# Performance work log

Hardware: AMD Instinct MI355X
Metric: run time of the kernel (lower is better)

## Reference

```python
import jax, jax.numpy as jnp
import numpy as np

EMBED_DIM = 768
NUM_HEADS = 12
HEAD_DIM = EMBED_DIM // NUM_HEADS
SCALE = HEAD_DIM ** -0.5


def setup_inputs() -> dict:
    key = jax.random.key(0)
    k_x, k_qkv, k_pw, k_pb = jax.random.split(key, 4)
    B, N = 2, 4096
    x = jax.random.normal(k_x, (B, N, EMBED_DIM), dtype=jnp.float32)
    # nn.Linear weights stored as [out, in]; we keep [in, out] for x @ W
    w_qkv = jax.random.normal(k_qkv, (EMBED_DIM, 3 * EMBED_DIM), dtype=jnp.float32) * (EMBED_DIM ** -0.5)
    w_proj = jax.random.normal(k_pw, (EMBED_DIM, EMBED_DIM), dtype=jnp.float32) * (EMBED_DIM ** -0.5)
    b_proj = jax.random.normal(k_pb, (EMBED_DIM,), dtype=jnp.float32) * 0.02
    return {"x": x, "w_qkv": w_qkv, "w_proj": w_proj, "b_proj": b_proj}


def reference(x, w_qkv, w_proj, b_proj):
    B, N, D = x.shape
    H, hd = NUM_HEADS, HEAD_DIM
    qkv = x @ w_qkv                                   # [B, N, 3*D]
    qkv = qkv.reshape(B, N, 3, H, hd)                 # matches '(qkv h d)' split order
    q, k, v = (qkv[:, :, i].transpose(0, 2, 1, 3) for i in range(3))  # each [B, H, N, hd]
    attn = jnp.einsum('bhid,bhjd->bhij', q, k) * SCALE  # [B, H, N, N] fully materialized
    attn = jax.nn.softmax(attn, axis=-1)
    out = jnp.einsum('bhij,bhjd->bhid', attn, v)        # [B, H, N, hd]
    out = out.transpose(0, 2, 1, 3).reshape(B, N, D)    # 'b h n d -> b n (h d)'
    return out @ w_proj + b_proj
```

## Files before the change

### kernel.cpp

```cpp
#include <hip/hip_runtime.h>
#include <hip/hip_bf16.h>

typedef __attribute__((ext_vector_type(4))) float f32x4;
typedef __attribute__((ext_vector_type(4))) int i32x4;
typedef __attribute__((ext_vector_type(8))) short s16x8;

static constexpr int NB = 2, NH = 12, SEQ = 4096, DM = 768, HD = 64;
static constexpr int ROWS = NB * SEQ;
static constexpr float QSC = 0.125f * 1.44269504f;

#define MFMA(a, b, c) __builtin_amdgcn_mfma_f32_16x16x32_bf16((a), (b), (c), 0, 0, 0)

typedef const void __attribute__((address_space(1)))* gas_t;
typedef void __attribute__((address_space(3)))* las_t;

__device__ __forceinline__ short f2bf(float f) {
  union { float f; unsigned u; } v; v.f = f;
  unsigned r = v.u + 0x7fffu + ((v.u >> 16) & 1u);
  return (short)(r >> 16);
}

__device__ __forceinline__ float exp2v(float x) {
  float r; asm("v_exp_f32 %0, %1" : "=v"(r) : "v"(x)); return r;
}

__global__ __launch_bounds__(256) void k_cast4(const float* __restrict__ in,
                                               short* __restrict__ out, int n4) {
  int i = blockIdx.x * 256 + threadIdx.x;
  if (i < n4) {
    float4 v = reinterpret_cast<const float4*>(in)[i];
    short4 o = { f2bf(v.x), f2bf(v.y), f2bf(v.z), f2bf(v.w) };
    reinterpret_cast<short4*>(out)[i] = o;
  }
}

__global__ __launch_bounds__(256) void k_tcast2(const float* __restrict__ in,
                                                short* __restrict__ out, int r, int c) {
  __shared__ short tile[32][33];
  int tpc = c >> 5;
  int by = blockIdx.x / tpc, bx = blockIdx.x % tpc;
  int tx = threadIdx.x & 31, ty = threadIdx.x >> 5;
#pragma unroll
  for (int i = 0; i < 4; ++i)
    tile[ty + i * 8][tx] = f2bf(in[(size_t)(by * 32 + ty + i * 8) * c + bx * 32 + tx]);
  __syncthreads();
#pragma unroll
  for (int i = 0; i < 4; ++i)
    out[(size_t)(bx * 32 + ty + i * 8) * r + by * 32 + tx] = tile[tx][ty + i * 8];
}

__device__ __forceinline__ void gemm128(const short* __restrict__ A,
                                        const short* __restrict__ Bt,
                                        int K, int row0, int col0,
                                        short As[2][4096], short Bs[2][4096],
                                        f32x4 acc[4][4]) {
  int w = threadIdx.x >> 6, l = threadIdx.x & 63;
  int q = l & 15, g = l >> 4;
  int wr = w >> 1, wc = w & 1;
  int sr = w * 16 + (l >> 2);
  int sc = (l & 3) * 8;

#define STG(buf, k0)                                                           \
  {                                                                            \
    _Pragma("unroll")                                                          \
    for (int i = 0; i < 2; ++i) {                                              \
      __builtin_amdgcn_global_load_lds(                                        \
          (gas_t)(A + (size_t)(row0 + i * 64 + sr) * K + (k0) + sc),           \
          (las_t)&As[buf][i * 2048 + w * 512], 16, 0, 0);                      \
      __builtin_amdgcn_global_load_lds(                                        \
          (gas_t)(Bt + (size_t)(col0 + i * 64 + sr) * K + (k0) + sc),          \
          (las_t)&Bs[buf][i * 2048 + w * 512], 16, 0, 0);                      \
    }                                                                          \
  }

  STG(0, 0);
  __syncthreads();
  int cur = 0;
  for (int k0 = 0; k0 < K; k0 += 32) {
    if (k0 + 32 < K) STG(cur ^ 1, k0 + 32);
    s16x8 af[4], bf[4];
#pragma unroll
    for (int m = 0; m < 4; ++m)
      af[m] = *reinterpret_cast<const s16x8*>(&As[cur][(wr * 64 + m * 16 + q) * 32 + g * 8]);
#pragma unroll
    for (int n = 0; n < 4; ++n)
      bf[n] = *reinterpret_cast<const s16x8*>(&Bs[cur][(wc * 64 + n * 16 + q) * 32 + g * 8]);
#pragma unroll
    for (int m = 0; m < 4; ++m)
#pragma unroll
      for (int n = 0; n < 4; ++n)
        acc[m][n] = MFMA(af[m], bf[n], acc[m][n]);
    __syncthreads();
    cur ^= 1;
  }
#undef STG
}

__global__ __launch_bounds__(256) void k_gemm_qkv2(const short* __restrict__ xb,
                                                   const short* __restrict__ wt,
                                                   short* __restrict__ qw,
                                                   short* __restrict__ kw,
                                                   short* __restrict__ vtw) {
  __shared__ __align__(16) short As[2][4096], Bs[2][4096];
  int bid = blockIdx.x;
  int swz = (bid & 7) * 144 + (bid >> 3);
  int brow = swz / 18, bcol = swz % 18;
  int row0 = brow * 128, col0 = bcol * 128;
  f32x4 acc[4][4] = {};
  gemm128(xb, wt, DM, row0, col0, As, Bs, acc);

  int w = threadIdx.x >> 6, l = threadIdx.x & 63;
  int q = l & 15, g = l >> 4;
  int wr = w >> 1, wc = w & 1;
  int cb = col0 + wc * 64;
  int which = cb / DM, h = (cb % DM) >> 6;
  int rowb = row0 + wr * 64;
  int b = rowb >> 12;
  int bh = b * NH + h;
#pragma unroll
  for (int m = 0; m < 4; ++m) {
#pragma unroll
    for (int n = 0; n < 4; ++n) {
      int d = n * 16 + q;
      if (which == 2) {
        int nseq = (rowb & 4095) + m * 16 + g * 4;
        short4 ov = { f2bf(acc[m][n][0]), f2bf(acc[m][n][1]),
                      f2bf(acc[m][n][2]), f2bf(acc[m][n][3]) };
        *reinterpret_cast<short4*>(&vtw[((size_t)bh * HD + d) * SEQ + nseq]) = ov;
      } else {
        short* dst = (which == 0) ? qw : kw;
        float sc = (which == 0) ? QSC : 1.f;
#pragma unroll
        for (int r = 0; r < 4; ++r) {
          int nseq = (rowb & 4095) + m * 16 + g * 4 + r;
          dst[((size_t)bh * SEQ + nseq) * HD + d] = f2bf(acc[m][n][r] * sc);
        }
      }
    }
  }
}

__global__ __launch_bounds__(256) void k_gemm_proj2(const short* __restrict__ aob,
                                                    const short* __restrict__ wt,
                                                    const float* __restrict__ bias,
                                                    float* __restrict__ out) {
  __shared__ __align__(16) short As[2][4096], Bs[2][4096];
  int bid = blockIdx.x;
  int swz = (bid & 7) * 48 + (bid >> 3);
  int brow = swz / 6, bcol = swz % 6;
  int row0 = brow * 128, col0 = bcol * 128;
  f32x4 acc[4][4] = {};
  gemm128(aob, wt, DM, row0, col0, As, Bs, acc);

  int w = threadIdx.x >> 6, l = threadIdx.x & 63;
  int q = l & 15, g = l >> 4;
  int wr = w >> 1, wc = w & 1;
#pragma unroll
  for (int m = 0; m < 4; ++m)
#pragma unroll
    for (int n = 0; n < 4; ++n) {
      int col = col0 + wc * 64 + n * 16 + q;
      float bv = bias[col];
#pragma unroll
      for (int r = 0; r < 4; ++r) {
        int row = row0 + wr * 64 + m * 16 + g * 4 + r;
        out[(size_t)row * DM + col] = acc[m][n][r] + bv;
      }
    }
}

__global__ __launch_bounds__(256, 4) void k_attn7(const short* __restrict__ qw,
                                                  const short* __restrict__ kw,
                                                  const short* __restrict__ vtw,
                                                  short* __restrict__ ao) {
  __shared__ __align__(16) short lds[2][2][4096];

  int bid = blockIdx.x;
  int swz = (bid & 7) * 96 + (bid >> 3);
  int bh = swz >> 5;
  int qchunk = swz & 31;

  int w = threadIdx.x >> 6, l = threadIdx.x & 63;
  int q = l & 15, g = l >> 4;

  const short* Kg = kw + (size_t)bh * SEQ * HD;
  const short* Vg = vtw + (size_t)bh * HD * SEQ;

  int ss = (l & 7) ^ (l >> 3) ^ ((w & 1) << 2);
  int rst = w * 8 + (l >> 3);

  int qbase = qchunk * 128 + w * 32;
  s16x8 qf[2][2];
#pragma unroll
  for (int qt2 = 0; qt2 < 2; ++qt2)
#pragma unroll
    for (int kh = 0; kh < 2; ++kh)
      qf[qt2][kh] = *reinterpret_cast<const s16x8*>(
          qw + ((size_t)bh * SEQ + qbase + qt2 * 16 + q) * HD + kh * 32 + g * 8);

  s16x8 ones;
  {
    short o1 = (q == 0) ? (short)0x3F80 : (short)0;
#pragma unroll
    for (int i = 0; i < 8; ++i) ones[i] = o1;
  }

  f32x4 o[2][4] = {};
  f32x4 lsa[2] = {};

#define STAGE(buf, t)                                                              \
  {                                                                                \
    int key0 = (t) * 64;                                                           \
    _Pragma("unroll")                                                              \
    for (int i = 0; i < 2; ++i) {                                                  \
      const short* gk = Kg + (size_t)(key0 + i * 32 + rst) * HD + ss * 8;          \
      __builtin_amdgcn_global_load_lds((gas_t)gk,                                  \
          (las_t)&lds[buf][0][i * 2048 + w * 512], 16, 0, 0);                      \
      const short* gv = Vg + (size_t)(i * 32 + rst) * SEQ + key0 + ss * 8;         \
      __builtin_amdgcn_global_load_lds((gas_t)gv,                                  \
          (las_t)&lds[buf][1][i * 2048 + w * 512], 16, 0, 0);                      \
    }                                                                              \
  }

  STAGE(0, 0);
  __syncthreads();
  int cur = 0;

  for (int t = 0; t < SEQ / 64; ++t) {
    if (t + 1 < SEQ / 64) {
      if (cur) STAGE(0, t + 1) else STAGE(1, t + 1)
    }
    const short* Kl = &lds[cur][0][0];
    const short* Vl = &lds[cur][1][0];

    f32x4 s[2][2][2] = {};
    __builtin_amdgcn_s_setprio(1);
#pragma unroll
    for (int c = 0; c < 2; ++c)
#pragma unroll
      for (int ab = 0; ab < 2; ++ab) {
        int R = c * 32 + ab * 4 + ((q >> 2) << 3) + (q & 3);
        int sw = (R & 7) ^ (((R >> 3) & 1) << 2);
#pragma unroll
        for (int kh = 0; kh < 2; ++kh) {
          int slot = (kh * 4 + g) ^ sw;
          s16x8 af = *reinterpret_cast<const s16x8*>(Kl + R * 64 + slot * 8);
          s[c][ab][0] = MFMA(af, qf[0][kh], s[c][ab][0]);
          s[c][ab][1] = MFMA(af, qf[1][kh], s[c][ab][1]);
        }
      }
    __builtin_amdgcn_s_setprio(0);

    i32x4 pv[2][2];
#pragma unroll
    for (int qt2 = 0; qt2 < 2; ++qt2) {
      unsigned u[16];
#define SV(i) s[(i) >> 3][((i) >> 2) & 1][qt2][(i) & 3]
#pragma unroll
      for (int i = 0; i < 16; ++i)
        u[i] = __float_as_uint(exp2v(SV(i)));
#undef SV
#pragma unroll
      for (int c = 0; c < 2; ++c)
#pragma unroll
        for (int j = 0; j < 4; ++j)
          pv[c][qt2][j] = (int)__builtin_amdgcn_perm(u[c * 8 + 2 * j + 1],
                                                     u[c * 8 + 2 * j], 0x07060302u);
    }

    __builtin_amdgcn_s_setprio(1);
#pragma unroll
    for (int c = 0; c < 2; ++c) {
      s16x8 p0 = __builtin_bit_cast(s16x8, pv[c][0]);
      s16x8 p1 = __builtin_bit_cast(s16x8, pv[c][1]);
#pragma unroll
      for (int dt = 0; dt < 4; ++dt) {
        int R = dt * 16 + q;
        int sw = (R & 7) ^ (((R >> 3) & 1) << 2);
        int slot = (c * 4 + g) ^ sw;
        s16x8 vf = *reinterpret_cast<const s16x8*>(Vl + R * 64 + slot * 8);
        o[0][dt] = MFMA(vf, p0, o[0][dt]);
        o[1][dt] = MFMA(vf, p1, o[1][dt]);
      }
      lsa[0] = MFMA(ones, p0, lsa[0]);
      lsa[1] = MFMA(ones, p1, lsa[1]);
    }
    __builtin_amdgcn_s_setprio(0);

    __syncthreads();
    cur ^= 1;
  }
#undef STAGE

  int b = bh / NH, h = bh % NH;
  float ls0 = __shfl(lsa[0][0], q);
  float ls1 = __shfl(lsa[1][0], q);
  float inv[2] = { 1.f / ls0, 1.f / ls1 };
#pragma unroll
  for (int qt2 = 0; qt2 < 2; ++qt2) {
    size_t row = (size_t)b * SEQ + qbase + qt2 * 16 + q;
    short* op = ao + row * DM + h * HD;
#pragma unroll
    for (int dt = 0; dt < 4; ++dt) {
      short4 ov = { f2bf(o[qt2][dt][0] * inv[qt2]), f2bf(o[qt2][dt][1] * inv[qt2]),
                    f2bf(o[qt2][dt][2] * inv[qt2]), f2bf(o[qt2][dt][3] * inv[qt2]) };
      *reinterpret_cast<short4*>(op + dt * 16 + g * 4) = ov;
    }
  }
}

extern "C" void kernel_launch(void* const* d_in, const int* in_sizes, int n_in,
                              void* d_out, int out_size, void* d_ws, size_t ws_size,
                              hipStream_t stream) {
  const float* x      = (const float*)d_in[0];
  const float* w_qkv  = (const float*)d_in[1];
  const float* w_proj = (const float*)d_in[2];
  const float* b_proj = (const float*)d_in[3];
  float* out = (float*)d_out;

  char* p = (char*)d_ws;
  auto take = [&](size_t bytes) { char* r = p; p += (bytes + 255) & ~(size_t)255; return r; };
  short* xb     = (short*)take((size_t)ROWS * DM * 2);
  short* wtqkv  = (short*)take((size_t)3 * DM * DM * 2);
  short* wtproj = (short*)take((size_t)DM * DM * 2);
  short* qw     = (short*)take((size_t)NB * NH * SEQ * HD * 2);
  short* kw     = (short*)take((size_t)NB * NH * SEQ * HD * 2);
  short* vtw    = (short*)take((size_t)NB * NH * HD * SEQ * 2);
  short* ao     = (short*)take((size_t)ROWS * DM * 2);

  int n4 = ROWS * DM / 4;
  k_cast4<<<(n4 + 255) / 256, 256, 0, stream>>>(x, xb, n4);
  k_tcast2<<<(DM / 32) * (3 * DM / 32), 256, 0, stream>>>(w_qkv, wtqkv, DM, 3 * DM);
  k_tcast2<<<(DM / 32) * (DM / 32), 256, 0, stream>>>(w_proj, wtproj, DM, DM);
  k_gemm_qkv2<<<64 * 18, 256, 0, stream>>>(xb, wtqkv, qw, kw, vtw);
  k_attn7<<<NB * NH * (SEQ / 128), 256, 0, stream>>>(qw, kw, vtw, ao);
  k_gemm_proj2<<<64 * 6, 256, 0, stream>>>(ao, wtproj, b_proj, out);
}
```

Measured before the change: 180.9 us.

## Split attention key range across two blocks and merge partials in a separate kernel

Each attention block now processes only half of the key sequence, which doubles the grid so more blocks can run concurrently on the CUs. Each block writes unnormalized fp32 partial outputs and row sums to a workspace. A new merge kernel adds the two halves, normalizes them and writes the bf16 attention output. This trades better CU occupancy for extra fp32 global traffic and an additional kernel launch.

Measured after the change: 190.7 us. 1.05x slower.

```diff
diff --git a/kernel.cpp b/kernel.cpp
--- a/kernel.cpp
+++ b/kernel.cpp
@@ -7,6 +7,7 @@
 
 static constexpr int NB = 2, NH = 12, SEQ = 4096, DM = 768, HD = 64;
 static constexpr int ROWS = NB * SEQ;
+static constexpr int BHROWS = NB * NH * SEQ;
 static constexpr float QSC = 0.125f * 1.44269504f;
 
 #define MFMA(a, b, c) __builtin_amdgcn_mfma_f32_16x16x32_bf16((a), (b), (c), 0, 0, 0)
@@ -169,16 +170,19 @@
     }
 }
 
-__global__ __launch_bounds__(256, 4) void k_attn7(const short* __restrict__ qw,
-                                                  const short* __restrict__ kw,
-                                                  const short* __restrict__ vtw,
-                                                  short* __restrict__ ao) {
+__global__ __launch_bounds__(256, 4) void k_attn11(const short* __restrict__ qw,
+                                                   const short* __restrict__ kw,
+                                                   const short* __restrict__ vtw,
+                                                   float* __restrict__ opart,
+                                                   float* __restrict__ lpart) {
   __shared__ __align__(16) short lds[2][2][4096];
 
   int bid = blockIdx.x;
-  int swz = (bid & 7) * 96 + (bid >> 3);
-  int bh = swz >> 5;
-  int qchunk = swz & 31;
+  int swz = (bid & 7) * 192 + (bid >> 3);
+  int bh = swz >> 6;
+  int rem = swz & 63;
+  int qchunk = rem >> 1;
+  int half = rem & 1;
 
   int w = threadIdx.x >> 6, l = threadIdx.x & 63;
   int q = l & 15, g = l >> 4;
@@ -188,6 +192,7 @@
 
   int ss = (l & 7) ^ (l >> 3) ^ ((w & 1) << 2);
   int rst = w * 8 + (l >> 3);
+  int kbase = half * (SEQ / 2);
 
   int qbase = qchunk * 128 + w * 32;
   s16x8 qf[2][2];
@@ -210,7 +215,7 @@
 
 #define STAGE(buf, t)                                                              \
   {                                                                                \
-    int key0 = (t) * 64;                                                           \
+    int key0 = kbase + (t) * 64;                                                   \
     _Pragma("unroll")                                                              \
     for (int i = 0; i < 2; ++i) {                                                  \
       const short* gk = Kg + (size_t)(key0 + i * 32 + rst) * HD + ss * 8;          \
@@ -226,8 +231,8 @@
   __syncthreads();
   int cur = 0;
 
-  for (int t = 0; t < SEQ / 64; ++t) {
-    if (t + 1 < SEQ / 64) {
+  for (int t = 0; t < SEQ / 128; ++t) {
+    if (t + 1 < SEQ / 128) {
       if (cur) STAGE(0, t + 1) else STAGE(1, t + 1)
     }
     const short* Kl = &lds[cur][0][0];
@@ -292,21 +297,41 @@
   }
 #undef STAGE
 
-  int b = bh / NH, h = bh % NH;
   float ls0 = __shfl(lsa[0][0], q);
   float ls1 = __shfl(lsa[1][0], q);
-  float inv[2] = { 1.f / ls0, 1.f / ls1 };
 #pragma unroll
   for (int qt2 = 0; qt2 < 2; ++qt2) {
-    size_t row = (size_t)b * SEQ + qbase + qt2 * 16 + q;
-    short* op = ao + row * DM + h * HD;
-#pragma unroll
-    for (int dt = 0; dt < 4; ++dt) {
-      short4 ov = { f2bf(o[qt2][dt][0] * inv[qt2]), f2bf(o[qt2][dt][1] * inv[qt2]),
-                    f2bf(o[qt2][dt][2] * inv[qt2]), f2bf(o[qt2][dt][3] * inv[qt2]) };
-      *reinterpret_cast<short4*>(op + dt * 16 + g * 4) = ov;
-    }
-  }
+    size_t prow = (size_t)bh * SEQ + qbase + qt2 * 16 + q;
+    float* op = opart + ((size_t)half * BHROWS + prow) * HD;
+#pragma unroll
+    for (int dt = 0; dt < 4; ++dt)
+      *reinterpret_cast<f32x4*>(op + dt * 16 + g * 4) = o[qt2][dt];
+  }
+  if (g == 0) {
+    size_t prow0 = (size_t)bh * SEQ + qbase + q;
+    lpart[(size_t)half * BHROWS + prow0] = ls0;
+    lpart[(size_t)half * BHROWS + prow0 + 16] = ls1;
+  }
+}
+
+__global__ __launch_bounds__(256) void k_merge(const float* __restrict__ opart,
+                                               const float* __restrict__ lpart,
+                                               short* __restrict__ ao) {
+  int i = blockIdx.x * 256 + threadIdx.x;
+  if (i >= BHROWS * HD / 4) return;
+  int bhn = i >> 4;
+  int d4 = (i & 15) * 4;
+  const float* p0 = opart + (size_t)bhn * HD + d4;
+  const float* p1 = p0 + (size_t)BHROWS * HD;
+  f32x4 a = *reinterpret_cast<const f32x4*>(p0);
+  f32x4 b = *reinterpret_cast<const f32x4*>(p1);
+  float inv = 1.f / (lpart[bhn] + lpart[BHROWS + bhn]);
+  int bh = bhn >> 12, n = bhn & 4095;
+  int bb = bh / NH, h = bh % NH;
+  short* op = ao + ((size_t)(bb * SEQ + n)) * DM + h * HD + d4;
+  short4 ov = { f2bf((a[0] + b[0]) * inv), f2bf((a[1] + b[1]) * inv),
+                f2bf((a[2] + b[2]) * inv), f2bf((a[3] + b[3]) * inv) };
+  *reinterpret_cast<short4*>(op) = ov;
 }
 
 extern "C" void kernel_launch(void* const* d_in, const int* in_sizes, int n_in,
@@ -327,12 +352,15 @@
   short* kw     = (short*)take((size_t)NB * NH * SEQ * HD * 2);
   short* vtw    = (short*)take((size_t)NB * NH * HD * SEQ * 2);
   short* ao     = (short*)take((size_t)ROWS * DM * 2);
+  float* opart  = (float*)take((size_t)2 * BHROWS * HD * 4);
+  float* lpart  = (float*)take((size_t)2 * BHROWS * 4);
 
   int n4 = ROWS * DM / 4;
   k_cast4<<<(n4 + 255) / 256, 256, 0, stream>>>(x, xb, n4);
   k_tcast2<<<(DM / 32) * (3 * DM / 32), 256, 0, stream>>>(w_qkv, wtqkv, DM, 3 * DM);
   k_tcast2<<<(DM / 32) * (DM / 32), 256, 0, stream>>>(w_proj, wtproj, DM, DM);
   k_gemm_qkv2<<<64 * 18, 256, 0, stream>>>(xb, wtqkv, qw, kw, vtw);
-  k_attn7<<<NB * NH * (SEQ / 128), 256, 0, stream>>>(qw, kw, vtw, ao);
+  k_attn11<<<NB * NH * (SEQ / 128) * 2, 256, 0, stream>>>(qw, kw, vtw, opart, lpart);
+  k_merge<<<(BHROWS * HD / 4 + 255) / 256, 256, 0, stream>>>(opart, lpart, ao);
   k_gemm_proj2<<<64 * 6, 256, 0, stream>>>(ao, wtproj, b_proj, out);
 }
```
